# Kernel tuning notes

Measured on AMD Instinct MI355X. Metric: run time of the kernel, lower is better.

The kernel has to match this reference:

```python
import jax, jax.numpy as jnp
import numpy as np

D_MODEL = 512
N_HEADS = 8
D_K = D_MODEL // N_HEADS
B, L = 4, 2048


def setup_inputs() -> dict:
    key = jax.random.key(0)
    ks = jax.random.split(key, 9)
    s = 1.0 / np.sqrt(D_MODEL)  # nn.Linear default init scale (uniform bound)
    def lin(kw, kb):
        W = jax.random.uniform(kw, (D_MODEL, D_MODEL), jnp.float32, -s, s)
        b = jax.random.uniform(kb, (D_MODEL,), jnp.float32, -s, s)
        return W, b
    Wq, bq = lin(ks[0], ks[1])
    Wk, bk = lin(ks[2], ks[3])
    Wv, bv = lin(ks[4], ks[5])
    return {
        "queries": jax.random.normal(ks[6], (B, L, D_MODEL), jnp.float32),
        "keys": jax.random.normal(ks[7], (B, L, D_MODEL), jnp.float32),
        "values": jax.random.normal(ks[8], (B, L, D_MODEL), jnp.float32),
        "Wq": Wq, "bq": bq, "Wk": Wk, "bk": bk, "Wv": Wv, "bv": bv,
    }


def reference(queries, keys, values, Wq, bq, Wk, bk, Wv, bv):
    # Torch Linear: y = x @ W.T + b; here W stored as [in, out] so y = x @ W + b
    Bsz, Lq, _ = queries.shape
    Lk = keys.shape[1]
    # project and split heads -> [B, H, L, d_k]
    Q = (queries @ Wq + bq).reshape(Bsz, Lq, N_HEADS, D_K).transpose(0, 2, 1, 3)
    K = (keys @ Wk + bk).reshape(Bsz, Lk, N_HEADS, D_K).transpose(0, 2, 1, 3)
    V = (values @ Wv + bv).reshape(Bsz, Lk, N_HEADS, D_K).transpose(0, 2, 1, 3)
    scores = jnp.einsum("bhqd,bhkd->bhqk", Q, K) / np.sqrt(D_K).astype(np.float32)
    attn_weights = jax.nn.softmax(scores, axis=-1)  # dropout is identity in eval
    out = jnp.einsum("bhqk,bhkd->bhqd", attn_weights, V)
    out = out.transpose(0, 2, 1, 3).reshape(Bsz, Lq, D_MODEL)
    return out, attn_weights
```

## Files before the change

kernel.cpp:

```cpp
#include <hip/hip_runtime.h>
#include <hip/hip_bf16.h>


using u16 = unsigned short;
using u32 = unsigned int;

typedef __attribute__((ext_vector_type(4))) float  f32x4;
typedef __attribute__((ext_vector_type(8))) short  s16x8;
typedef __attribute__((ext_vector_type(2))) unsigned int u32x2;
typedef __attribute__((ext_vector_type(4))) unsigned int u32x4;

#define MFMA16(a,b,c) __builtin_amdgcn_mfma_f32_16x16x32_bf16(a,b,c,0,0,0)

__device__ __forceinline__ u16 f2bf(float f){
  u32 x; __builtin_memcpy(&x, &f, 4);
  x += 0x7FFFu + ((x >> 16) & 1u);
  return (u16)(x >> 16);
}
__device__ __forceinline__ u32 pk2(float a, float b){
  return (u32)f2bf(a) | ((u32)f2bf(b) << 16);
}
#if __has_builtin(__builtin_amdgcn_exp2f)
__device__ __forceinline__ float ex2(float x){ return __builtin_amdgcn_exp2f(x); }
#else
__device__ __forceinline__ float ex2(float x){ return exp2f(x); }
#endif

#define SCALE2 0.18033688f

__global__ void wt_kernel(const float* __restrict__ W0, const float* __restrict__ W1,
                          const float* __restrict__ W2,
                          u16* __restrict__ T0, u16* __restrict__ T1, u16* __restrict__ T2){
  const float* W = blockIdx.z==0 ? W0 : (blockIdx.z==1 ? W1 : W2);
  u16*         T = blockIdx.z==0 ? T0 : (blockIdx.z==1 ? T1 : T2);
  __shared__ u16 t[32][33];
  int x = threadIdx.x, y0 = threadIdx.y;
  int bx = blockIdx.x*32, by = blockIdx.y*32;
  #pragma unroll
  for (int i=0;i<4;i++){ int y=y0+i*8; t[y][x] = f2bf(W[(by+y)*512 + bx + x]); }
  __syncthreads();
  #pragma unroll
  for (int i=0;i<4;i++){ int y=y0+i*8; T[(bx+y)*512 + by + x] = t[x][y]; }
}

__global__ __launch_bounds__(256,2) void proj_kernel(
    const float* __restrict__ q_in, const float* __restrict__ k_in, const float* __restrict__ v_in,
    const u16* __restrict__ Wt,
    const float* __restrict__ bq, const float* __restrict__ bk, const float* __restrict__ bv,
    u16* __restrict__ Qo, u16* __restrict__ Ko, u16* __restrict__ Vto)
{
  const int mode = blockIdx.z;
  const int lt = blockIdx.x;
  const int nt = blockIdx.y;
  const float* Xf   = mode==0 ? q_in : (mode==1 ? k_in : v_in);
  const u16*   Wm   = Wt + (size_t)mode*512*512;
  const float* bias = mode==0 ? bq : (mode==1 ? bk : bv);

  __shared__ __align__(16) u16 As[128*32];
  __shared__ __align__(16) u16 Bs[128*32];

  u16* Wdst = (mode<2) ? As : Bs;
  u16* Xdst = (mode<2) ? Bs : As;
  const int wrow0 = nt*128, xrow0 = lt*128;

  const int t = threadIdx.x;
  const int w = t>>6, lane = t&63, l16 = lane&15, quad = lane>>4;
  const int am = (w&1)*64, bn = (w>>1)*64;

  f32x4 acc[4][4];
  #pragma unroll
  for (int i=0;i<4;i++)
    #pragma unroll
    for (int j=0;j<4;j++) acc[i][j] = (f32x4){0.f,0.f,0.f,0.f};

  for (int kk=0; kk<512; kk+=32){
    __syncthreads();
    #pragma unroll
    for (int j=0;j<2;j++){
      int id = j*256 + t;
      int row = id>>2, c4 = id&3;
      int sw = c4 ^ (row&3) ^ ((row>>2)&3);
      u32x4 vw = *(const u32x4*)(Wm + (size_t)(wrow0+row)*512 + kk + c4*8);
      *(u32x4*)((char*)Wdst + row*64 + sw*16) = vw;
      const float* xp = Xf + (size_t)(xrow0+row)*512 + kk + c4*8;
      f32x4 x0 = *(const f32x4*)xp;
      f32x4 x1 = *(const f32x4*)(xp+4);
      u32x4 vx = { pk2(x0[0],x0[1]), pk2(x0[2],x0[3]),
                   pk2(x1[0],x1[1]), pk2(x1[2],x1[3]) };
      *(u32x4*)((char*)Xdst + row*64 + sw*16) = vx;
    }
    __syncthreads();
    s16x8 fa[4], fb[4];
    #pragma unroll
    for (int i=0;i<4;i++){
      int ra = am + i*16 + l16;
      fa[i] = *(const s16x8*)((const char*)As + ra*64 + ((quad ^ (ra&3) ^ ((ra>>2)&3))*16));
      int rb = bn + i*16 + l16;
      fb[i] = *(const s16x8*)((const char*)Bs + rb*64 + ((quad ^ (rb&3) ^ ((rb>>2)&3))*16));
    }
    #pragma unroll
    for (int i=0;i<4;i++)
      #pragma unroll
      for (int j=0;j<4;j++)
        acc[i][j] = MFMA16(fa[i], fb[j], acc[i][j]);
  }

  if (mode < 2){
    u16* Out = mode==0 ? Qo : Ko;
    #pragma unroll
    for (int i=0;i<4;i++){
      int n0 = nt*128 + am + i*16 + quad*4;
      float b4[4];
      #pragma unroll
      for (int r=0;r<4;r++) b4[r] = bias[n0+r];
      int h = n0>>6, d0 = n0&63;
      #pragma unroll
      for (int j=0;j<4;j++){
        int lg = lt*128 + bn + j*16 + l16;
        int b = lg>>11, ll = lg&2047;
        u32x2 pk = { pk2(acc[i][j][0]+b4[0], acc[i][j][1]+b4[1]),
                     pk2(acc[i][j][2]+b4[2], acc[i][j][3]+b4[3]) };
        *(u32x2*)(Out + ((size_t)(((b<<3)+h)*2048 + ll)<<6) + d0) = pk;
      }
    }
  } else {
    #pragma unroll
    for (int j=0;j<4;j++){
      int nv = nt*128 + bn + j*16 + l16;
      float bvv = bias[nv];
      int h = nv>>6, d = nv&63;
      #pragma unroll
      for (int i=0;i<4;i++){
        int lg = lt*128 + am + i*16 + quad*4;
        int b = lg>>11, ll = lg&2047;
        u32x2 pk = { pk2(acc[i][j][0]+bvv, acc[i][j][1]+bvv),
                     pk2(acc[i][j][2]+bvv, acc[i][j][3]+bvv) };
        *(u32x2*)(Vto + ((size_t)(((b<<3)+h)*64 + d)<<11) + ll) = pk;
      }
    }
  }
}

__global__ __launch_bounds__(256,2) void attn_kernel(
    const u16* __restrict__ Q, const u16* __restrict__ K, const u16* __restrict__ Vt,
    float* __restrict__ out, float* __restrict__ attn)
{
  const int qt = blockIdx.x;
  const int bh = blockIdx.z*8 + blockIdx.y;
  const int q0 = qt*128;
  const u16* Qg = Q  + (size_t)bh*2048*64;
  const u16* Kg = K  + (size_t)bh*2048*64;
  const u16* Vg = Vt + (size_t)bh*64*2048;
  float* attng = attn + ((size_t)bh*2048 + q0)*2048;

  __shared__ __align__(128) char smem[65536];
  u16*   Qs = (u16*)smem;
  u16*   Vs = (u16*)(smem + 16384);
  u16*   Ks = (u16*)(smem + 32768);
  u16*   Ws = (u16*)(smem + 32768);
  float* Ls = (float*)(smem + 49152);

  const int t = threadIdx.x;
  const int w = t>>6, lane = t&63, l16 = lane&15, quad = lane>>4;
  const int coff = (w&1)*64, roff = (w>>1)*64;

  if (t < 128) Ls[t] = 0.f;

  #pragma unroll
  for (int j=0;j<4;j++){
    int id = j*256 + t; int row = id>>3, ch = id&7;
    u32x4 v = *(const u32x4*)(Qg + (size_t)(q0+row)*64 + ch*8);
    *(u32x4*)((char*)Qs + row*128 + ((ch ^ (row&7))*16)) = v;
  }

  float lsum[4] = {0.f,0.f,0.f,0.f};

  for (int kt=0; kt<16; kt++){
    __syncthreads();
    #pragma unroll
    for (int j=0;j<4;j++){
      int id = j*256 + t; int row = id>>3, ch = id&7;
      u32x4 v = *(const u32x4*)(Kg + (size_t)(kt*128+row)*64 + ch*8);
      *(u32x4*)((char*)Ks + row*128 + ((ch ^ (row&7))*16)) = v;
    }
    __syncthreads();
    f32x4 s[4][4];
    #pragma unroll
    for (int ci=0;ci<4;ci++)
      #pragma unroll
      for (int ri=0;ri<4;ri++) s[ci][ri] = (f32x4){0.f,0.f,0.f,0.f};
    #pragma unroll
    for (int kc=0;kc<2;kc++){
      s16x8 fa[4], fb[4];
      #pragma unroll
      for (int i=0;i<4;i++){
        int rc = coff + i*16 + l16;
        fa[i] = *(const s16x8*)((const char*)Ks + rc*128 + (((kc*4+quad) ^ (rc&7))*16));
        int rr = roff + i*16 + l16;
        fb[i] = *(const s16x8*)((const char*)Qs + rr*128 + (((kc*4+quad) ^ (rr&7))*16));
      }
      #pragma unroll
      for (int ci=0;ci<4;ci++)
        #pragma unroll
        for (int ri=0;ri<4;ri++)
          s[ci][ri] = MFMA16(fa[ci], fb[ri], s[ci][ri]);
    }
    #pragma unroll
    for (int ri=0;ri<4;ri++){
      float ps = 0.f;
      #pragma unroll
      for (int ci=0;ci<4;ci++)
        #pragma unroll
        for (int r=0;r<4;r++) ps += ex2(s[ci][ri][r]*SCALE2);
      lsum[ri] += ps;
    }
  }
  #pragma unroll
  for (int ri=0;ri<4;ri++){
    float v = lsum[ri];
    v += __shfl_xor(v, 16, 64);
    v += __shfl_xor(v, 32, 64);
    lsum[ri] = v;
  }
  if (quad == 0){
    #pragma unroll
    for (int ri=0;ri<4;ri++) atomicAdd(&Ls[roff + ri*16 + l16], lsum[ri]);
  }
  __syncthreads();
  float rinv[4];
  #pragma unroll
  for (int ri=0;ri<4;ri++) rinv[ri] = 1.0f / Ls[roff + ri*16 + l16];

  f32x4 o[2][4];
  #pragma unroll
  for (int mi=0;mi<2;mi++)
    #pragma unroll
    for (int ni=0;ni<4;ni++) o[mi][ni] = (f32x4){0.f,0.f,0.f,0.f};

  for (int kt=0; kt<16; kt++){
    __syncthreads();
    #pragma unroll
    for (int j=0;j<4;j++){
      int id = j*256 + t; int row = id>>3, ch = id&7;
      u32x4 v = *(const u32x4*)(Kg + (size_t)(kt*128+row)*64 + ch*8);
      *(u32x4*)((char*)Ks + row*128 + ((ch ^ (row&7))*16)) = v;
    }
    #pragma unroll
    for (int j=0;j<4;j++){
      int id = j*256 + t; int row = id>>4, ch = id&15;
      u32x4 v = *(const u32x4*)(Vg + (size_t)row*2048 + kt*128 + ch*8);
      *(u32x4*)((char*)Vs + row*256 + ((ch ^ (row&15))*16)) = v;
    }
    __syncthreads();
    f32x4 s[4][4];
    #pragma unroll
    for (int ci=0;ci<4;ci++)
      #pragma unroll
      for (int ri=0;ri<4;ri++) s[ci][ri] = (f32x4){0.f,0.f,0.f,0.f};
    #pragma unroll
    for (int kc=0;kc<2;kc++){
      s16x8 fa[4], fb[4];
      #pragma unroll
      for (int i=0;i<4;i++){
        int rc = coff + i*16 + l16;
        fa[i] = *(const s16x8*)((const char*)Ks + rc*128 + (((kc*4+quad) ^ (rc&7))*16));
        int rr = roff + i*16 + l16;
        fb[i] = *(const s16x8*)((const char*)Qs + rr*128 + (((kc*4+quad) ^ (rr&7))*16));
      }
      #pragma unroll
      for (int ci=0;ci<4;ci++)
        #pragma unroll
        for (int ri=0;ri<4;ri++)
          s[ci][ri] = MFMA16(fa[ci], fb[ri], s[ci][ri]);
    }
    __syncthreads();
    #pragma unroll
    for (int ci=0;ci<4;ci++){
      #pragma unroll
      for (int ri=0;ri<4;ri++){
        f32x4 e;
        e[0] = ex2(s[ci][ri][0]*SCALE2)*rinv[ri];
        e[1] = ex2(s[ci][ri][1]*SCALE2)*rinv[ri];
        e[2] = ex2(s[ci][ri][2]*SCALE2)*rinv[ri];
        e[3] = ex2(s[ci][ri][3]*SCALE2)*rinv[ri];
        int rr = roff + ri*16 + l16;
        int c0 = coff + ci*16 + quad*4;
        *(f32x4*)(attng + (size_t)rr*2048 + kt*128 + c0) = e;
        u32x2 pk = { pk2(e[0], e[1]), pk2(e[2], e[3]) };
        *(u32x2*)((char*)Ws + rr*256 + (((c0>>3) ^ (rr&15))*16) + (c0&7)*2) = pk;
      }
    }
    __syncthreads();
    #pragma unroll
    for (int kc=0;kc<4;kc++){
      s16x8 wa[2], vb[4];
      #pragma unroll
      for (int mi=0;mi<2;mi++){
        int rr = w*32 + mi*16 + l16;
        wa[mi] = *(const s16x8*)((const char*)Ws + rr*256 + (((kc*4+quad) ^ (rr&15))*16));
      }
      #pragma unroll
      for (int ni=0;ni<4;ni++){
        int dd = ni*16 + l16;
        vb[ni] = *(const s16x8*)((const char*)Vs + dd*256 + (((kc*4+quad) ^ (dd&15))*16));
      }
      #pragma unroll
      for (int mi=0;mi<2;mi++)
        #pragma unroll
        for (int ni=0;ni<4;ni++)
          o[mi][ni] = MFMA16(wa[mi], vb[ni], o[mi][ni]);
    }
  }

  float* og = out + ((size_t)(bh>>3)*2048 + q0)*512 + (bh&7)*64;
  #pragma unroll
  for (int mi=0;mi<2;mi++){
    #pragma unroll
    for (int ni=0;ni<4;ni++){
      int dd = ni*16 + l16;
      #pragma unroll
      for (int r=0;r<4;r++){
        int rr = w*32 + mi*16 + quad*4 + r;
        og[(size_t)rr*512 + dd] = o[mi][ni][r];
      }
    }
  }
}

extern "C" void kernel_launch(void* const* d_in, const int* in_sizes, int n_in,
                              void* d_out, int out_size, void* d_ws, size_t ws_size,
                              hipStream_t stream) {
  (void)in_sizes; (void)n_in; (void)out_size; (void)ws_size;
  const float* q_in = (const float*)d_in[0];
  const float* k_in = (const float*)d_in[1];
  const float* v_in = (const float*)d_in[2];
  const float* Wq   = (const float*)d_in[3];
  const float* bq   = (const float*)d_in[4];
  const float* Wk   = (const float*)d_in[5];
  const float* bk   = (const float*)d_in[6];
  const float* Wv   = (const float*)d_in[7];
  const float* bv   = (const float*)d_in[8];

  u16* ws  = (u16*)d_ws;
  u16* Wt  = ws;
  u16* Qw  = ws + 786432;
  u16* Kw  = Qw + 4194304;
  u16* Vtw = Kw + 4194304;

  float* outp  = (float*)d_out;
  float* attnp = outp + 4194304;

  wt_kernel  <<<dim3(16,16,3), dim3(32,8), 0, stream>>>(Wq, Wk, Wv, Wt, Wt+262144, Wt+524288);
  proj_kernel<<<dim3(64,4,3),  256,       0, stream>>>(q_in, k_in, v_in, Wt, bq, bk, bv, Qw, Kw, Vtw);
  attn_kernel<<<dim3(16,8,4),  256,       0, stream>>>(Qw, Kw, Vtw, outp, attnp);
}
```

Before: 730.4 us.

## Restructure attention kernel with 512 threads, async double-buffered K/V, register-resident P

Doubles the attention block to 512 threads so each wave owns 32 query rows. Q fragments are held in registers, and the first softmax-sum pass reads K directly from global memory. The second pass double-buffers K/V tiles in LDS using global_load_lds async copies. The bf16 probabilities feed 16x16x16 MFMAs straight from registers instead of round-tripping through LDS, and partial outputs from the paired column-half waves are reduced through shared memory at the end. The aim is to remove per-tile synchronization and LDS staging costs; the risks are register pressure at 512 threads and reliance on async-copy semantics, since there is no explicit wait before the next tile is used.

```diff
diff --git a/kernel.cpp b/kernel.cpp
--- a/kernel.cpp
+++ b/kernel.cpp
@@ -7,10 +7,20 @@
 
 typedef __attribute__((ext_vector_type(4))) float  f32x4;
 typedef __attribute__((ext_vector_type(8))) short  s16x8;
+typedef __attribute__((ext_vector_type(4))) short  s16x4;
 typedef __attribute__((ext_vector_type(2))) unsigned int u32x2;
 typedef __attribute__((ext_vector_type(4))) unsigned int u32x4;
 
 #define MFMA16(a,b,c) __builtin_amdgcn_mfma_f32_16x16x32_bf16(a,b,c,0,0,0)
+
+#if __has_builtin(__builtin_amdgcn_mfma_f32_16x16x16bf16_1k)
+#define MFMA1616(a,b,c) __builtin_amdgcn_mfma_f32_16x16x16bf16_1k(a,b,c,0,0,0)
+#else
+__device__ __forceinline__ f32x4 MFMA1616(s16x4 a, s16x4 b, f32x4 c){
+  asm("v_mfma_f32_16x16x16_bf16 %0, %1, %2, %0" : "+v"(c) : "v"(a), "v"(b));
+  return c;
+}
+#endif
 
 __device__ __forceinline__ u16 f2bf(float f){
   u32 x; __builtin_memcpy(&x, &f, 4);
@@ -25,6 +35,16 @@
 #else
 __device__ __forceinline__ float ex2(float x){ return exp2f(x); }
 #endif
+
+__device__ __forceinline__ void async16(const u16* src, char* wavebase, int lane){
+#if __has_builtin(__builtin_amdgcn_global_load_lds)
+  __builtin_amdgcn_global_load_lds(
+      (const __attribute__((address_space(1))) unsigned int*)src,
+      (__attribute__((address_space(3))) unsigned int*)wavebase, 16, 0, 0);
+#else
+  *(u32x4*)(wavebase + lane*16) = *(const u32x4*)src;
+#endif
+}
 
 #define SCALE2 0.18033688f
 
@@ -141,7 +161,7 @@
   }
 }
 
-__global__ __launch_bounds__(256,2) void attn_kernel(
+__global__ __launch_bounds__(512,4) void attn_kernel(
     const u16* __restrict__ Q, const u16* __restrict__ K, const u16* __restrict__ Vt,
     float* __restrict__ out, float* __restrict__ attn)
 {
@@ -154,59 +174,53 @@
   float* attng = attn + ((size_t)bh*2048 + q0)*2048;
 
   __shared__ __align__(128) char smem[65536];
-  u16*   Qs = (u16*)smem;
-  u16*   Vs = (u16*)(smem + 16384);
-  u16*   Ks = (u16*)(smem + 32768);
-  u16*   Ws = (u16*)(smem + 32768);
   float* Ls = (float*)(smem + 49152);
+  float* Os = (float*)smem;
 
   const int t = threadIdx.x;
   const int w = t>>6, lane = t&63, l16 = lane&15, quad = lane>>4;
-  const int coff = (w&1)*64, roff = (w>>1)*64;
+  const int coff = (w&1)*64, roff = (w>>1)*32;
 
   if (t < 128) Ls[t] = 0.f;
-
-  #pragma unroll
-  for (int j=0;j<4;j++){
-    int id = j*256 + t; int row = id>>3, ch = id&7;
-    u32x4 v = *(const u32x4*)(Qg + (size_t)(q0+row)*64 + ch*8);
-    *(u32x4*)((char*)Qs + row*128 + ((ch ^ (row&7))*16)) = v;
-  }
-
-  float lsum[4] = {0.f,0.f,0.f,0.f};
-
+  __syncthreads();
+
+  s16x8 qf[2][2];
+  #pragma unroll
+  for (int kc=0;kc<2;kc++)
+    #pragma unroll
+    for (int ri=0;ri<2;ri++)
+      qf[kc][ri] = *(const s16x8*)(Qg + (size_t)(q0 + roff + ri*16 + l16)*64 + (kc*4+quad)*8);
+
+  #pragma unroll
+  for (int j=0;j<2;j++){
+    int id = j*512 + t; int row = id>>3, ch = id&7;
+    async16(Kg + (size_t)row*64 + ((ch ^ (row&7))*8), smem + (j*512 + w*64)*16, lane);
+  }
+  #pragma unroll
+  for (int j=0;j<2;j++){
+    int id = j*512 + t; int row = id>>4, ch = id&15;
+    async16(Vg + (size_t)row*2048 + ((ch ^ (row&15))*8), smem + 32768 + (j*512 + w*64)*16, lane);
+  }
+
+  float lsum[2] = {0.f, 0.f};
   for (int kt=0; kt<16; kt++){
-    __syncthreads();
-    #pragma unroll
-    for (int j=0;j<4;j++){
-      int id = j*256 + t; int row = id>>3, ch = id&7;
-      u32x4 v = *(const u32x4*)(Kg + (size_t)(kt*128+row)*64 + ch*8);
-      *(u32x4*)((char*)Ks + row*128 + ((ch ^ (row&7))*16)) = v;
-    }
-    __syncthreads();
-    f32x4 s[4][4];
+    f32x4 s[4][2];
     #pragma unroll
     for (int ci=0;ci<4;ci++)
       #pragma unroll
-      for (int ri=0;ri<4;ri++) s[ci][ri] = (f32x4){0.f,0.f,0.f,0.f};
+      for (int ri=0;ri<2;ri++) s[ci][ri] = (f32x4){0.f,0.f,0.f,0.f};
     #pragma unroll
     for (int kc=0;kc<2;kc++){
-      s16x8 fa[4], fb[4];
-      #pragma unroll
-      for (int i=0;i<4;i++){
-        int rc = coff + i*16 + l16;
-        fa[i] = *(const s16x8*)((const char*)Ks + rc*128 + (((kc*4+quad) ^ (rc&7))*16));
-        int rr = roff + i*16 + l16;
-        fb[i] = *(const s16x8*)((const char*)Qs + rr*128 + (((kc*4+quad) ^ (rr&7))*16));
-      }
-      #pragma unroll
-      for (int ci=0;ci<4;ci++)
-        #pragma unroll
-        for (int ri=0;ri<4;ri++)
-          s[ci][ri] = MFMA16(fa[ci], fb[ri], s[ci][ri]);
-    }
-    #pragma unroll
-    for (int ri=0;ri<4;ri++){
+      #pragma unroll
+      for (int ci=0;ci<4;ci++){
+        int rc = kt*128 + coff + ci*16 + l16;
+        s16x8 fa = *(const s16x8*)(Kg + (size_t)rc*64 + (kc*4+quad)*8);
+        #pragma unroll
+        for (int ri=0;ri<2;ri++) s[ci][ri] = MFMA16(fa, qf[kc][ri], s[ci][ri]);
+      }
+    }
+    #pragma unroll
+    for (int ri=0;ri<2;ri++){
       float ps = 0.f;
       #pragma unroll
       for (int ci=0;ci<4;ci++)
@@ -216,114 +230,113 @@
     }
   }
   #pragma unroll
-  for (int ri=0;ri<4;ri++){
+  for (int ri=0;ri<2;ri++){
     float v = lsum[ri];
     v += __shfl_xor(v, 16, 64);
     v += __shfl_xor(v, 32, 64);
-    lsum[ri] = v;
-  }
-  if (quad == 0){
-    #pragma unroll
-    for (int ri=0;ri<4;ri++) atomicAdd(&Ls[roff + ri*16 + l16], lsum[ri]);
-  }
-  __syncthreads();
-  float rinv[4];
-  #pragma unroll
-  for (int ri=0;ri<4;ri++) rinv[ri] = 1.0f / Ls[roff + ri*16 + l16];
+    if (quad == 0) atomicAdd(&Ls[roff + ri*16 + l16], v);
+  }
+  __syncthreads();
+  float rinv[2];
+  #pragma unroll
+  for (int ri=0;ri<2;ri++) rinv[ri] = 1.0f / Ls[roff + ri*16 + l16];
+  __syncthreads();
 
   f32x4 o[2][4];
   #pragma unroll
-  for (int mi=0;mi<2;mi++)
-    #pragma unroll
-    for (int ni=0;ni<4;ni++) o[mi][ni] = (f32x4){0.f,0.f,0.f,0.f};
-
+  for (int ri=0;ri<2;ri++)
+    #pragma unroll
+    for (int ni=0;ni<4;ni++) o[ri][ni] = (f32x4){0.f,0.f,0.f,0.f};
+
+  int cur = 0;
   for (int kt=0; kt<16; kt++){
-    __syncthreads();
-    #pragma unroll
-    for (int j=0;j<4;j++){
-      int id = j*256 + t; int row = id>>3, ch = id&7;
-      u32x4 v = *(const u32x4*)(Kg + (size_t)(kt*128+row)*64 + ch*8);
-      *(u32x4*)((char*)Ks + row*128 + ((ch ^ (row&7))*16)) = v;
-    }
-    #pragma unroll
-    for (int j=0;j<4;j++){
-      int id = j*256 + t; int row = id>>4, ch = id&15;
-      u32x4 v = *(const u32x4*)(Vg + (size_t)row*2048 + kt*128 + ch*8);
-      *(u32x4*)((char*)Vs + row*256 + ((ch ^ (row&15))*16)) = v;
-    }
-    __syncthreads();
-    f32x4 s[4][4];
+    char* Kc = smem + cur*16384;
+    char* Vc = smem + 32768 + cur*16384;
+    char* Kn = smem + (cur^1)*16384;
+    char* Vn = smem + 32768 + (cur^1)*16384;
+    if (kt < 15){
+      #pragma unroll
+      for (int j=0;j<2;j++){
+        int id = j*512 + t; int row = id>>3, ch = id&7;
+        async16(Kg + (size_t)((kt+1)*128+row)*64 + ((ch ^ (row&7))*8),
+                Kn + (j*512 + w*64)*16, lane);
+      }
+      #pragma unroll
+      for (int j=0;j<2;j++){
+        int id = j*512 + t; int row = id>>4, ch = id&15;
+        async16(Vg + (size_t)row*2048 + (kt+1)*128 + ((ch ^ (row&15))*8),
+                Vn + (j*512 + w*64)*16, lane);
+      }
+    }
+    f32x4 s[4][2];
     #pragma unroll
     for (int ci=0;ci<4;ci++)
       #pragma unroll
-      for (int ri=0;ri<4;ri++) s[ci][ri] = (f32x4){0.f,0.f,0.f,0.f};
+      for (int ri=0;ri<2;ri++) s[ci][ri] = (f32x4){0.f,0.f,0.f,0.f};
     #pragma unroll
     for (int kc=0;kc<2;kc++){
-      s16x8 fa[4], fb[4];
-      #pragma unroll
-      for (int i=0;i<4;i++){
-        int rc = coff + i*16 + l16;
-        fa[i] = *(const s16x8*)((const char*)Ks + rc*128 + (((kc*4+quad) ^ (rc&7))*16));
-        int rr = roff + i*16 + l16;
-        fb[i] = *(const s16x8*)((const char*)Qs + rr*128 + (((kc*4+quad) ^ (rr&7))*16));
-      }
-      #pragma unroll
-      for (int ci=0;ci<4;ci++)
-        #pragma unroll
-        for (int ri=0;ri<4;ri++)
-          s[ci][ri] = MFMA16(fa[ci], fb[ri], s[ci][ri]);
-    }
-    __syncthreads();
+      #pragma unroll
+      for (int ci=0;ci<4;ci++){
+        int rc = coff + ci*16 + l16;
+        s16x8 fa = *(const s16x8*)(Kc + rc*128 + (((kc*4+quad) ^ (rc&7))*16));
+        #pragma unroll
+        for (int ri=0;ri<2;ri++) s[ci][ri] = MFMA16(fa, qf[kc][ri], s[ci][ri]);
+      }
+    }
+    s16x4 pa[4][2];
     #pragma unroll
     for (int ci=0;ci<4;ci++){
       #pragma unroll
-      for (int ri=0;ri<4;ri++){
+      for (int ri=0;ri<2;ri++){
         f32x4 e;
-        e[0] = ex2(s[ci][ri][0]*SCALE2)*rinv[ri];
-        e[1] = ex2(s[ci][ri][1]*SCALE2)*rinv[ri];
-        e[2] = ex2(s[ci][ri][2]*SCALE2)*rinv[ri];
-        e[3] = ex2(s[ci][ri][3]*SCALE2)*rinv[ri];
+        #pragma unroll
+        for (int r=0;r<4;r++) e[r] = ex2(s[ci][ri][r]*SCALE2)*rinv[ri];
         int rr = roff + ri*16 + l16;
         int c0 = coff + ci*16 + quad*4;
         *(f32x4*)(attng + (size_t)rr*2048 + kt*128 + c0) = e;
-        u32x2 pk = { pk2(e[0], e[1]), pk2(e[2], e[3]) };
-        *(u32x2*)((char*)Ws + rr*256 + (((c0>>3) ^ (rr&15))*16) + (c0&7)*2) = pk;
-      }
-    }
-    __syncthreads();
-    #pragma unroll
-    for (int kc=0;kc<4;kc++){
-      s16x8 wa[2], vb[4];
-      #pragma unroll
-      for (int mi=0;mi<2;mi++){
-        int rr = w*32 + mi*16 + l16;
-        wa[mi] = *(const s16x8*)((const char*)Ws + rr*256 + (((kc*4+quad) ^ (rr&15))*16));
-      }
+        s16x4 p;
+        #pragma unroll
+        for (int r=0;r<4;r++) p[r] = (short)f2bf(e[r]);
+        pa[ci][ri] = p;
+      }
+    }
+    #pragma unroll
+    for (int cc=0;cc<4;cc++){
       #pragma unroll
       for (int ni=0;ni<4;ni++){
         int dd = ni*16 + l16;
-        vb[ni] = *(const s16x8*)((const char*)Vs + dd*256 + (((kc*4+quad) ^ (dd&15))*16));
-      }
-      #pragma unroll
-      for (int mi=0;mi<2;mi++)
-        #pragma unroll
-        for (int ni=0;ni<4;ni++)
-          o[mi][ni] = MFMA16(wa[mi], vb[ni], o[mi][ni]);
-    }
-  }
-
-  float* og = out + ((size_t)(bh>>3)*2048 + q0)*512 + (bh&7)*64;
-  #pragma unroll
-  for (int mi=0;mi<2;mi++){
-    #pragma unroll
-    for (int ni=0;ni<4;ni++){
-      int dd = ni*16 + l16;
-      #pragma unroll
-      for (int r=0;r<4;r++){
-        int rr = w*32 + mi*16 + quad*4 + r;
-        og[(size_t)rr*512 + dd] = o[mi][ni][r];
-      }
-    }
+        int ch = ((coff>>3) + cc*2 + (quad>>1)) ^ (dd&15);
+        s16x4 vb = *(const s16x4*)(Vc + dd*256 + ch*16 + (quad&1)*8);
+        #pragma unroll
+        for (int ri=0;ri<2;ri++) o[ri][ni] = MFMA1616(pa[cc][ri], vb, o[ri][ni]);
+      }
+    }
+    __syncthreads();
+    cur ^= 1;
+  }
+
+  if (w & 1){
+    #pragma unroll
+    for (int ri=0;ri<2;ri++)
+      #pragma unroll
+      for (int ni=0;ni<4;ni++)
+        #pragma unroll
+        for (int r=0;r<4;r++)
+          Os[(roff + ri*16 + quad*4 + r)*68 + ni*16 + l16] = o[ri][ni][r];
+  }
+  __syncthreads();
+  if (!(w & 1)){
+    float* og = out + ((size_t)(bh>>3)*2048 + q0)*512 + (bh&7)*64;
+    #pragma unroll
+    for (int ri=0;ri<2;ri++)
+      #pragma unroll
+      for (int ni=0;ni<4;ni++)
+        #pragma unroll
+        for (int r=0;r<4;r++){
+          int rr = roff + ri*16 + quad*4 + r;
+          int dd = ni*16 + l16;
+          og[(size_t)rr*512 + dd] = o[ri][ni][r] + Os[rr*68 + dd];
+        }
   }
 }
 
@@ -352,5 +365,5 @@
 
   wt_kernel  <<<dim3(16,16,3), dim3(32,8), 0, stream>>>(Wq, Wk, Wv, Wt, Wt+262144, Wt+524288);
   proj_kernel<<<dim3(64,4,3),  256,       0, stream>>>(q_in, k_in, v_in, Wt, bq, bk, bv, Qw, Kw, Vtw);
-  attn_kernel<<<dim3(16,8,4),  256,       0, stream>>>(Qw, Kw, Vtw, outp, attnp);
-}
+  attn_kernel<<<dim3(16,8,4),  512,       0, stream>>>(Qw, Kw, Vtw, outp, attnp);
+}
```

Measured after the change: 700.3 us. 1.04x faster.
